# Kernel tuning notes

Measured on AMD Instinct MI355X. Metric: run time of the kernel, lower is better.

The kernel has to match this reference:

```python
import jax, jax.numpy as jnp
import numpy as np

B, N, E, H, L = 1, 1024, 32, 1024, 8  # batch, num concepts, dim_edge, dim_hidden, stack_len


def setup_inputs() -> dict:
    key = jax.random.key(0)
    k = jax.random.split(key, 12)
    vision_feat = jax.random.normal(k[0], (B, 36, H), jnp.float32)   # unused by forward
    feat = jax.random.normal(k[1], (B, N - 1, N, E), jnp.float32)
    feat_edge = jax.random.normal(k[2], (B, 1, N, E), jnp.float32)
    c_i = jax.random.normal(k[3], (B, H), jnp.float32)
    relation_mask = jnp.ones((B, N), jnp.float32)                    # only its size is read
    att_stack = jax.random.uniform(k[4], (B, N, N, L), dtype=jnp.float32)
    sp = jax.random.uniform(k[5], (B, L), dtype=jnp.float32)
    stack_ptr = sp / jnp.sum(sp, axis=-1, keepdims=True)             # soft stack pointer
    mem_in = jax.random.normal(k[6], (B, H), jnp.float32)
    mono_mask = (jax.random.uniform(k[7], (B, N, N, 1)) > 0.5).astype(jnp.float32)
    cross_mask = jax.random.uniform(k[8], (E,), dtype=jnp.float32)
    w_c = jax.random.normal(k[9], (E, H), jnp.float32) / np.sqrt(H).astype(np.float32)
    b_c = jax.random.normal(k[10], (E,), jnp.float32) * 0.01
    return {"vision_feat": vision_feat, "feat": feat, "feat_edge": feat_edge,
            "c_i": c_i, "relation_mask": relation_mask, "att_stack": att_stack,
            "stack_ptr": stack_ptr, "mem_in": mem_in, "mono_mask": mono_mask,
            "cross_mask": cross_mask, "w_c": w_c, "b_c": b_c}


def reference(vision_feat, feat, feat_edge, c_i, relation_mask, att_stack,
              stack_ptr, mem_in, mono_mask, cross_mask, w_c, b_c):
    b = feat_edge.shape[0]
    # query = map_c(c_i).view(B,1,1,-1).expand_as(feat_edge)
    query = (c_i @ w_c.T + b_c).reshape(b, 1, 1, -1)
    query = jnp.broadcast_to(query, feat_edge.shape)                 # (B,1,N,E)
    I = jnp.concatenate([query, feat], axis=1)                       # (B,N,N,E)
    # Fusion: -(x-y)^2 + relu(x+y), feat_edge broadcasts over dim1
    elt_prod = -(I - feat_edge) ** 2 + jax.nn.relu(I + feat_edge)    # (B,N,N,E)
    weit_matrix = mono_mask * elt_prod                               # (B,N,N,E)
    # soft stack read + permute(0,2,1): att_in[b,y,x] = sum_l att_stack[b,x,y,l]*ptr[b,l]
    att_in = jnp.einsum('bxyl,bl->byx', att_stack, stack_ptr)        # (B,N,N)
    # (att_in @ weit_matrix) @ cross_mask, then permute(0,2,1).
    # Contract the edge dim first (mathematically identical by linearity).
    wv = jnp.einsum('bmye,e->bmy', weit_matrix, cross_mask)          # (B,N,N)
    att_out = jnp.einsum('bxy,bmy->bxm', att_in, wv)                 # (B,N,N)
    # max-normalize with detached norm clamped to >= 1
    norm = jax.lax.stop_gradient(jnp.max(att_out, axis=1, keepdims=True))
    norm = jnp.where(norm <= 1, jnp.ones_like(norm), norm)
    att_out = att_out / norm
    # soft stack write
    ptr = stack_ptr[:, None, None, :]                                # (B,1,1,L)
    att_stack_new = att_out[..., None] * ptr + att_stack * (1 - ptr) # (B,N,N,L)
    return att_stack_new, stack_ptr, jnp.zeros_like(mem_in)
```

## Files before the change

kernel.cpp:

```cpp
#include <hip/hip_runtime.h>
#include <math.h>

#define N 1024
#define E 32
#define L 8
#define NN ((size_t)N * N)

using short8 = __attribute__((ext_vector_type(8))) short;
using f32x4v = __attribute__((ext_vector_type(4))) float;

__device__ inline ushort2 split_bf16(float v) {
  unsigned ui = __float_as_uint(v);
  ushort h = (ushort)(ui >> 16);
  float hv = __uint_as_float((unsigned)h << 16);
  float r = v - hv;
  ushort l = (ushort)(__float_as_uint(r) >> 16);
  return make_ushort2(h, l);
}

__device__ inline void gload16(const void* g, void* l) {
  __builtin_amdgcn_global_load_lds(
      (const __attribute__((address_space(1))) unsigned int*)g,
      (__attribute__((address_space(3))) unsigned int*)l, 16, 0, 0);
}

__global__ __launch_bounds__(256) void k_wv(
    const float* __restrict__ feat, const float* __restrict__ fe,
    const float* __restrict__ mono, const float* __restrict__ cm,
    const float* __restrict__ c_i, const float* __restrict__ w_c,
    const float* __restrict__ b_c,
    ushort* __restrict__ wv_h, ushort* __restrict__ wv_l) {
  __shared__ __align__(16) float qsm[32];
  int tid = threadIdx.x;
  int b = blockIdx.x;
  int seg = tid & 7;
  int rl = tid >> 3;
  int gid = b * 32 + rl;
  int m = gid >> 10;
  int y = gid & (N - 1);
  if (b < 32) {
    float s = 0.f;
    for (int h = seg; h < N; h += 8) s += c_i[h] * w_c[rl * N + h];
    s += __shfl_down(s, 4, 8);
    s += __shfl_down(s, 2, 8);
    s += __shfl_down(s, 1, 8);
    if (seg == 0) qsm[rl] = s + b_c[rl];
    __syncthreads();
  }
  float4 a;
  if (m == 0) {
    a = *((const float4*)qsm + seg);
  } else {
    a = *(const float4*)(feat + ((size_t)(m - 1) * N + y) * E + seg * 4);
  }
  float4 f = *(const float4*)(fe + (size_t)y * E + seg * 4);
  float4 c = *(const float4*)(cm + seg * 4);
  float dx = a.x - f.x, dy = a.y - f.y, dz = a.z - f.z, dw = a.w - f.w;
  float s = c.x * (fmaxf(a.x + f.x, 0.f) - dx * dx)
          + c.y * (fmaxf(a.y + f.y, 0.f) - dy * dy)
          + c.z * (fmaxf(a.z + f.z, 0.f) - dz * dz)
          + c.w * (fmaxf(a.w + f.w, 0.f) - dw * dw);
  s += __shfl_down(s, 4, 8);
  s += __shfl_down(s, 2, 8);
  s += __shfl_down(s, 1, 8);
  if (seg == 0) {
    float v = mono[gid] * s;
    ushort2 hl = split_bf16(v);
    wv_h[gid] = hl.x;
    wv_l[gid] = hl.y;
  }
}

__global__ __launch_bounds__(256) void k_P(
    const float* __restrict__ att_stack, const float* __restrict__ ptr,
    ushort* __restrict__ Pt_h, ushort* __restrict__ Pt_l,
    float* __restrict__ out_tail) {
  __shared__ ushort Ts[2][64][66];
  int tid = threadIdx.x;
  int b = blockIdx.x;
  if (b < 256) {
    int j0 = (b >> 4) * 64;
    int i0 = (b & 15) * 64;
    float p0 = ptr[0], p1 = ptr[1], p2 = ptr[2], p3 = ptr[3];
    float p4 = ptr[4], p5 = ptr[5], p6 = ptr[6], p7 = ptr[7];
    int w = tid >> 6, lane = tid & 63;
    #pragma unroll 4
    for (int r = 0; r < 16; ++r) {
      int jl = r * 4 + w;
      int il = lane;
      const float4* a =
          (const float4*)(att_stack + ((size_t)(j0 + jl) * N + i0 + il) * L);
      float4 a0 = a[0], a1 = a[1];
      float s = a0.x * p0 + a0.y * p1 + a0.z * p2 + a0.w * p3
              + a1.x * p4 + a1.y * p5 + a1.z * p6 + a1.w * p7;
      ushort2 hl = split_bf16(s);
      Ts[0][il][jl] = hl.x;
      Ts[1][il][jl] = hl.y;
    }
    __syncthreads();
    int il = tid >> 2, c = tid & 3;
    size_t o = (size_t)(i0 + il) * N + j0 + c * 16;
    {
      const uint* sp = (const uint*)&Ts[0][il][c * 16];
      uint4 d0 = {sp[0], sp[1], sp[2], sp[3]};
      uint4 d1 = {sp[4], sp[5], sp[6], sp[7]};
      *(uint4*)&Pt_h[o] = d0;
      *(uint4*)&Pt_h[o + 8] = d1;
    }
    {
      const uint* sp = (const uint*)&Ts[1][il][c * 16];
      uint4 d0 = {sp[0], sp[1], sp[2], sp[3]};
      uint4 d1 = {sp[4], sp[5], sp[6], sp[7]};
      *(uint4*)&Pt_l[o] = d0;
      *(uint4*)&Pt_l[o + 8] = d1;
    }
  } else {
    if (tid < 8) out_tail[tid] = ptr[tid];
    for (int i = tid; i < N; i += 256) out_tail[8 + i] = 0.f;
  }
}

__global__ __launch_bounds__(256) void k_mm(
    const ushort* __restrict__ Pt_h, const ushort* __restrict__ Pt_l,
    const ushort* __restrict__ wv_h, const ushort* __restrict__ wv_l,
    float* __restrict__ Cp) {
  __shared__ ushort As[2][64][32];
  __shared__ ushort Bs[2][64][32];
  int tid = threadIdx.x;
  int lane = tid & 63, w = tid >> 6;
  int x0 = blockIdx.x * 64, m0 = blockIdx.y * 64;
  int kb = blockIdx.z * 256;
  int srow = w * 16 + (lane >> 2);
  int scol = (lane & 3) * 8;
  const ushort* gAh = Pt_h + (size_t)(x0 + srow) * N + kb + scol;
  const ushort* gAl = Pt_l + (size_t)(x0 + srow) * N + kb + scol;
  const ushort* gBh = wv_h + (size_t)(m0 + srow) * N + kb + scol;
  const ushort* gBl = wv_l + (size_t)(m0 + srow) * N + kb + scol;
  ushort* lAh = &As[0][w * 16][0];
  ushort* lAl = &As[1][w * 16][0];
  ushort* lBh = &Bs[0][w * 16][0];
  ushort* lBl = &Bs[1][w * 16][0];
  int fr = w * 16 + (lane & 15);
  int fk = (lane >> 4) * 8;
  int fn = lane & 15;
  f32x4v acc[4];
  #pragma unroll
  for (int t = 0; t < 4; ++t) acc[t] = (f32x4v){0.f, 0.f, 0.f, 0.f};
  for (int kt = 0; kt < 8; ++kt) {
    __syncthreads();
    gload16(gAh + kt * 32, lAh);
    gload16(gAl + kt * 32, lAl);
    gload16(gBh + kt * 32, lBh);
    gload16(gBl + kt * 32, lBl);
    __syncthreads();
    short8 Ah = *(const short8*)&As[0][fr][fk];
    short8 Al = *(const short8*)&As[1][fr][fk];
    #pragma unroll
    for (int t = 0; t < 4; ++t) {
      short8 Bh = *(const short8*)&Bs[0][t * 16 + fn][fk];
      short8 Bl = *(const short8*)&Bs[1][t * 16 + fn][fk];
      acc[t] = __builtin_amdgcn_mfma_f32_16x16x32_bf16(Ah, Bh, acc[t], 0, 0, 0);
      acc[t] = __builtin_amdgcn_mfma_f32_16x16x32_bf16(Ah, Bl, acc[t], 0, 0, 0);
      acc[t] = __builtin_amdgcn_mfma_f32_16x16x32_bf16(Al, Bh, acc[t], 0, 0, 0);
    }
  }
  float* Cc = Cp + (size_t)blockIdx.z * NN;
  int orow = x0 + w * 16 + (lane >> 4) * 4;
  int ocol = m0 + fn;
  #pragma unroll
  for (int t = 0; t < 4; ++t)
    #pragma unroll
    for (int r = 0; r < 4; ++r)
      Cc[(size_t)(orow + r) * N + ocol + t * 16] = acc[t][r];
}

__global__ __launch_bounds__(1024) void k_rednorm(
    const float* __restrict__ Cp, float* __restrict__ C,
    float* __restrict__ normp) {
  int m = threadIdx.x;
  int xg = blockIdx.x;
  float mx = -INFINITY;
  #pragma unroll
  for (int j = 0; j < 4; ++j) {
    size_t idx = (size_t)(xg * 4 + j) * N + m;
    float s = Cp[idx] + Cp[idx + NN] + Cp[idx + 2 * NN] + Cp[idx + 3 * NN];
    C[idx] = s;
    mx = fmaxf(mx, s);
  }
  normp[(size_t)xg * N + m] = mx;
}

__global__ __launch_bounds__(256) void k_norm2(
    const float* __restrict__ normp, float* __restrict__ norm) {
  int m = blockIdx.x * 256 + threadIdx.x;
  float mx = -INFINITY;
  #pragma unroll 8
  for (int xg = 0; xg < 256; ++xg)
    mx = fmaxf(mx, normp[(size_t)xg * N + m]);
  norm[m] = (mx <= 1.f) ? 1.f : mx;
}

__global__ __launch_bounds__(256) void k_blend(
    const float* __restrict__ C, const float* __restrict__ norm,
    const float* __restrict__ att_stack, const float* __restrict__ ptr,
    float* __restrict__ out) {
  int gid = blockIdx.x * 256 + threadIdx.x;
  int m = gid & (N - 1);
  float a = C[gid] / norm[m];
  const float4* s = (const float4*)(att_stack + (size_t)gid * L);
  float4 s0 = s[0], s1 = s[1];
  float p0 = ptr[0], p1 = ptr[1], p2 = ptr[2], p3 = ptr[3];
  float p4 = ptr[4], p5 = ptr[5], p6 = ptr[6], p7 = ptr[7];
  float4 o0, o1;
  o0.x = a * p0 + s0.x * (1.f - p0);
  o0.y = a * p1 + s0.y * (1.f - p1);
  o0.z = a * p2 + s0.z * (1.f - p2);
  o0.w = a * p3 + s0.w * (1.f - p3);
  o1.x = a * p4 + s1.x * (1.f - p4);
  o1.y = a * p5 + s1.y * (1.f - p5);
  o1.z = a * p6 + s1.z * (1.f - p6);
  o1.w = a * p7 + s1.w * (1.f - p7);
  float4* o = (float4*)(out + (size_t)gid * L);
  o[0] = o0;
  o[1] = o1;
}

extern "C" void kernel_launch(void* const* d_in, const int* in_sizes, int n_in,
                              void* d_out, int out_size, void* d_ws, size_t ws_size,
                              hipStream_t stream) {
  const float* feat      = (const float*)d_in[1];
  const float* feat_edge = (const float*)d_in[2];
  const float* c_i       = (const float*)d_in[3];
  const float* att_stack = (const float*)d_in[5];
  const float* stack_ptr = (const float*)d_in[6];
  const float* mono_mask = (const float*)d_in[8];
  const float* cross_mask= (const float*)d_in[9];
  const float* w_c       = (const float*)d_in[10];
  const float* b_c       = (const float*)d_in[11];

  float* out = (float*)d_out;

  ushort* wv_h = (ushort*)d_ws;
  ushort* wv_l = wv_h + NN;
  ushort* Pt_h = wv_l + NN;
  ushort* Pt_l = Pt_h + NN;
  float*  Cp   = (float*)(Pt_l + NN);
  float*  C    = Cp + 4 * NN;
  float*  normp= C + NN;
  float*  norm = normp + (size_t)256 * N;

  float* out_tail = out + NN * L;

  k_wv<<<32768, 256, 0, stream>>>(feat, feat_edge, mono_mask, cross_mask,
                                  c_i, w_c, b_c, wv_h, wv_l);
  k_P<<<257, 256, 0, stream>>>(att_stack, stack_ptr, Pt_h, Pt_l, out_tail);
  dim3 mmgrid(16, 16, 4);
  k_mm<<<mmgrid, 256, 0, stream>>>(Pt_h, Pt_l, wv_h, wv_l, Cp);
  k_rednorm<<<256, 1024, 0, stream>>>(Cp, C, normp);
  k_norm2<<<4, 256, 0, stream>>>(normp, norm);
  k_blend<<<4096, 256, 0, stream>>>(C, norm, att_stack, stack_ptr, out);
}
```

Before: 321.6 us.

## Drop split-K in matmul and fuse column-max reduction into its epilogue

The matmul kernel no longer splits K four ways into partial buffers. Each block now runs the full K loop, writes C directly and computes a per-block column max in shared memory, which removes the separate reduce kernel and its 4xNN partial traffic. The wv kernel is also coarsened so each block handles four row groups (8192 blocks instead of 32768), with the query projection computed only by the first 8 blocks. The cost is fewer matmul blocks (256) with longer serial K loops, which reduces parallelism across the GPU.

```diff
diff --git a/kernel.cpp b/kernel.cpp
--- a/kernel.cpp
+++ b/kernel.cpp
@@ -35,39 +35,46 @@
   int b = blockIdx.x;
   int seg = tid & 7;
   int rl = tid >> 3;
-  int gid = b * 32 + rl;
-  int m = gid >> 10;
-  int y = gid & (N - 1);
-  if (b < 32) {
+  bool qblock = (b < 8);
+  if (qblock) {
+    int e = tid >> 3, r = tid & 7;
     float s = 0.f;
-    for (int h = seg; h < N; h += 8) s += c_i[h] * w_c[rl * N + h];
+    for (int h = r; h < N; h += 8) s += c_i[h] * w_c[e * N + h];
     s += __shfl_down(s, 4, 8);
     s += __shfl_down(s, 2, 8);
     s += __shfl_down(s, 1, 8);
-    if (seg == 0) qsm[rl] = s + b_c[rl];
-    __syncthreads();
-  }
-  float4 a;
-  if (m == 0) {
-    a = *((const float4*)qsm + seg);
-  } else {
-    a = *(const float4*)(feat + ((size_t)(m - 1) * N + y) * E + seg * 4);
-  }
-  float4 f = *(const float4*)(fe + (size_t)y * E + seg * 4);
+    if (r == 0) qsm[e] = s + b_c[e];
+    __syncthreads();
+  }
   float4 c = *(const float4*)(cm + seg * 4);
-  float dx = a.x - f.x, dy = a.y - f.y, dz = a.z - f.z, dw = a.w - f.w;
-  float s = c.x * (fmaxf(a.x + f.x, 0.f) - dx * dx)
-          + c.y * (fmaxf(a.y + f.y, 0.f) - dy * dy)
-          + c.z * (fmaxf(a.z + f.z, 0.f) - dz * dz)
-          + c.w * (fmaxf(a.w + f.w, 0.f) - dw * dw);
-  s += __shfl_down(s, 4, 8);
-  s += __shfl_down(s, 2, 8);
-  s += __shfl_down(s, 1, 8);
-  if (seg == 0) {
-    float v = mono[gid] * s;
-    ushort2 hl = split_bf16(v);
-    wv_h[gid] = hl.x;
-    wv_l[gid] = hl.y;
+  float4 qa;
+  if (qblock) qa = *((const float4*)qsm + seg);
+  #pragma unroll
+  for (int it = 0; it < 4; ++it) {
+    int gid = b * 128 + it * 32 + rl;
+    int m = gid >> 10;
+    int y = gid & (N - 1);
+    float4 a;
+    if (qblock) {
+      a = qa;
+    } else {
+      a = *(const float4*)(feat + ((size_t)(m - 1) * N + y) * E + seg * 4);
+    }
+    float4 f = *(const float4*)(fe + (size_t)y * E + seg * 4);
+    float dx = a.x - f.x, dy = a.y - f.y, dz = a.z - f.z, dw = a.w - f.w;
+    float s = c.x * (fmaxf(a.x + f.x, 0.f) - dx * dx)
+            + c.y * (fmaxf(a.y + f.y, 0.f) - dy * dy)
+            + c.z * (fmaxf(a.z + f.z, 0.f) - dz * dz)
+            + c.w * (fmaxf(a.w + f.w, 0.f) - dw * dw);
+    s += __shfl_down(s, 4, 8);
+    s += __shfl_down(s, 2, 8);
+    s += __shfl_down(s, 1, 8);
+    if (seg == 0) {
+      float v = mono[gid] * s;
+      ushort2 hl = split_bf16(v);
+      wv_h[gid] = hl.x;
+      wv_l[gid] = hl.y;
+    }
   }
 }
 
@@ -98,17 +105,17 @@
       Ts[1][il][jl] = hl.y;
     }
     __syncthreads();
-    int il = tid >> 2, c = tid & 3;
-    size_t o = (size_t)(i0 + il) * N + j0 + c * 16;
+    int il = tid >> 2, cc = tid & 3;
+    size_t o = (size_t)(i0 + il) * N + j0 + cc * 16;
     {
-      const uint* sp = (const uint*)&Ts[0][il][c * 16];
+      const uint* sp = (const uint*)&Ts[0][il][cc * 16];
       uint4 d0 = {sp[0], sp[1], sp[2], sp[3]};
       uint4 d1 = {sp[4], sp[5], sp[6], sp[7]};
       *(uint4*)&Pt_h[o] = d0;
       *(uint4*)&Pt_h[o + 8] = d1;
     }
     {
-      const uint* sp = (const uint*)&Ts[1][il][c * 16];
+      const uint* sp = (const uint*)&Ts[1][il][cc * 16];
       uint4 d0 = {sp[0], sp[1], sp[2], sp[3]};
       uint4 d1 = {sp[4], sp[5], sp[6], sp[7]};
       *(uint4*)&Pt_l[o] = d0;
@@ -123,19 +130,19 @@
 __global__ __launch_bounds__(256) void k_mm(
     const ushort* __restrict__ Pt_h, const ushort* __restrict__ Pt_l,
     const ushort* __restrict__ wv_h, const ushort* __restrict__ wv_l,
-    float* __restrict__ Cp) {
+    float* __restrict__ C, float* __restrict__ normp) {
   __shared__ ushort As[2][64][32];
   __shared__ ushort Bs[2][64][32];
+  __shared__ float nm[64][17];
   int tid = threadIdx.x;
   int lane = tid & 63, w = tid >> 6;
   int x0 = blockIdx.x * 64, m0 = blockIdx.y * 64;
-  int kb = blockIdx.z * 256;
   int srow = w * 16 + (lane >> 2);
   int scol = (lane & 3) * 8;
-  const ushort* gAh = Pt_h + (size_t)(x0 + srow) * N + kb + scol;
-  const ushort* gAl = Pt_l + (size_t)(x0 + srow) * N + kb + scol;
-  const ushort* gBh = wv_h + (size_t)(m0 + srow) * N + kb + scol;
-  const ushort* gBl = wv_l + (size_t)(m0 + srow) * N + kb + scol;
+  const ushort* gAh = Pt_h + (size_t)(x0 + srow) * N + scol;
+  const ushort* gAl = Pt_l + (size_t)(x0 + srow) * N + scol;
+  const ushort* gBh = wv_h + (size_t)(m0 + srow) * N + scol;
+  const ushort* gBl = wv_l + (size_t)(m0 + srow) * N + scol;
   ushort* lAh = &As[0][w * 16][0];
   ushort* lAl = &As[1][w * 16][0];
   ushort* lBh = &Bs[0][w * 16][0];
@@ -146,7 +153,7 @@
   f32x4v acc[4];
   #pragma unroll
   for (int t = 0; t < 4; ++t) acc[t] = (f32x4v){0.f, 0.f, 0.f, 0.f};
-  for (int kt = 0; kt < 8; ++kt) {
+  for (int kt = 0; kt < 32; ++kt) {
     __syncthreads();
     gload16(gAh + kt * 32, lAh);
     gload16(gAl + kt * 32, lAl);
@@ -164,38 +171,35 @@
       acc[t] = __builtin_amdgcn_mfma_f32_16x16x32_bf16(Al, Bh, acc[t], 0, 0, 0);
     }
   }
-  float* Cc = Cp + (size_t)blockIdx.z * NN;
   int orow = x0 + w * 16 + (lane >> 4) * 4;
   int ocol = m0 + fn;
-  #pragma unroll
-  for (int t = 0; t < 4; ++t)
+  int cidx = w * 4 + (lane >> 4);
+  #pragma unroll
+  for (int t = 0; t < 4; ++t) {
+    float mx = -INFINITY;
     #pragma unroll
-    for (int r = 0; r < 4; ++r)
-      Cc[(size_t)(orow + r) * N + ocol + t * 16] = acc[t][r];
-}
-
-__global__ __launch_bounds__(1024) void k_rednorm(
-    const float* __restrict__ Cp, float* __restrict__ C,
-    float* __restrict__ normp) {
-  int m = threadIdx.x;
-  int xg = blockIdx.x;
-  float mx = -INFINITY;
-  #pragma unroll
-  for (int j = 0; j < 4; ++j) {
-    size_t idx = (size_t)(xg * 4 + j) * N + m;
-    float s = Cp[idx] + Cp[idx + NN] + Cp[idx + 2 * NN] + Cp[idx + 3 * NN];
-    C[idx] = s;
-    mx = fmaxf(mx, s);
-  }
-  normp[(size_t)xg * N + m] = mx;
+    for (int r = 0; r < 4; ++r) {
+      float v = acc[t][r];
+      C[(size_t)(orow + r) * N + ocol + t * 16] = v;
+      mx = fmaxf(mx, v);
+    }
+    nm[t * 16 + fn][cidx] = mx;
+  }
+  __syncthreads();
+  if (tid < 64) {
+    float mx = nm[tid][0];
+    #pragma unroll
+    for (int j = 1; j < 16; ++j) mx = fmaxf(mx, nm[tid][j]);
+    normp[(size_t)blockIdx.x * N + m0 + tid] = mx;
+  }
 }
 
 __global__ __launch_bounds__(256) void k_norm2(
     const float* __restrict__ normp, float* __restrict__ norm) {
   int m = blockIdx.x * 256 + threadIdx.x;
-  float mx = -INFINITY;
-  #pragma unroll 8
-  for (int xg = 0; xg < 256; ++xg)
+  float mx = normp[m];
+  #pragma unroll
+  for (int xg = 1; xg < 16; ++xg)
     mx = fmaxf(mx, normp[(size_t)xg * N + m]);
   norm[m] = (mx <= 1.f) ? 1.f : mx;
 }
@@ -244,19 +248,17 @@
   ushort* wv_l = wv_h + NN;
   ushort* Pt_h = wv_l + NN;
   ushort* Pt_l = Pt_h + NN;
-  float*  Cp   = (float*)(Pt_l + NN);
-  float*  C    = Cp + 4 * NN;
+  float*  C    = (float*)(Pt_l + NN);
   float*  normp= C + NN;
-  float*  norm = normp + (size_t)256 * N;
+  float*  norm = normp + (size_t)16 * N;
 
   float* out_tail = out + NN * L;
 
-  k_wv<<<32768, 256, 0, stream>>>(feat, feat_edge, mono_mask, cross_mask,
-                                  c_i, w_c, b_c, wv_h, wv_l);
+  k_wv<<<8192, 256, 0, stream>>>(feat, feat_edge, mono_mask, cross_mask,
+                                 c_i, w_c, b_c, wv_h, wv_l);
   k_P<<<257, 256, 0, stream>>>(att_stack, stack_ptr, Pt_h, Pt_l, out_tail);
-  dim3 mmgrid(16, 16, 4);
-  k_mm<<<mmgrid, 256, 0, stream>>>(Pt_h, Pt_l, wv_h, wv_l, Cp);
-  k_rednorm<<<256, 1024, 0, stream>>>(Cp, C, normp);
+  dim3 mmgrid(16, 16);
+  k_mm<<<mmgrid, 256, 0, stream>>>(Pt_h, Pt_l, wv_h, wv_l, C, normp);
   k_norm2<<<4, 256, 0, stream>>>(normp, norm);
   k_blend<<<4096, 256, 0, stream>>>(C, norm, att_stack, stack_ptr, out);
 }
```

New measurement: 291.1 us. -9.5%, faster.
